# Performance work log

Measured on AMD Instinct MI355X. Metric: run time of the kernel, lower is better.

The kernel has to match this reference:

```python
import jax, jax.numpy as jnp
from jax import lax
import numpy as np

T, N, C, S = 256, 64, 7356, 32
NEG = -1e9  # finite stand-in for -inf (keeps grads clean)


def setup_inputs() -> dict:
    key = jax.random.key(0)
    k1, k2, k3 = jax.random.split(key, 3)
    out = jax.random.normal(k1, (T, N, C), dtype=jnp.float32)
    # PyTorch CTCLoss expects log-probs; the module passes `out` through as-is,
    # so we feed log_softmax'd activations (what the surrounding model produces).
    out = jax.nn.log_softmax(out, axis=-1)
    text = jax.random.randint(k2, (N, S), 1, C)            # labels in [1, C-1], blank=0 excluded
    pre_len = jnp.full((N,), T, dtype=jnp.int64 if jax.config.jax_enable_x64 else jnp.int32)
    lengths = jax.random.randint(k3, (N,), 16, S + 1)       # target lengths in [16, 32]
    return {"out": out, "text": text, "pre_len": pre_len, "lengths": lengths}


def _ctc_loss_mean(logp, targets, input_lengths, target_lengths):
    # logp: [T, N, C] log-probs; targets: [N, S]; lengths: [N]
    Tt, Nn, _ = logp.shape
    Ss = targets.shape[1]
    L = 2 * Ss + 1
    # Extended label sequence: blank, l1, blank, l2, ..., blank
    ext = jnp.zeros((Nn, L), dtype=targets.dtype).at[:, 1::2].set(targets)  # [N, L]
    ext_m2 = jnp.concatenate([jnp.zeros((Nn, 2), dtype=ext.dtype), ext[:, :-2]], axis=1)
    skip = (jnp.arange(L)[None, :] >= 2) & (ext != 0) & (ext != ext_m2)      # [N, L]

    # Gather per-frame log-probs of extended labels: [T, N, L]
    lp_ext = logp[:, jnp.arange(Nn)[:, None], ext]

    alpha0 = jnp.full((Nn, L), NEG, dtype=logp.dtype)
    alpha0 = alpha0.at[:, 0].set(lp_ext[0, :, 0]).at[:, 1].set(lp_ext[0, :, 1])

    negcol1 = jnp.full((Nn, 1), NEG, dtype=logp.dtype)
    negcol2 = jnp.full((Nn, 2), NEG, dtype=logp.dtype)

    def step(alpha, lp_t):
        s1 = jnp.concatenate([negcol1, alpha[:, :-1]], axis=1)
        s2 = jnp.concatenate([negcol2, alpha[:, :-2]], axis=1)
        a = jnp.logaddexp(alpha, s1)
        a = jnp.logaddexp(a, jnp.where(skip, s2, NEG))
        new = a + lp_t
        return new, new

    _, alphas_rest = lax.scan(step, alpha0, lp_ext[1:])
    alphas = jnp.concatenate([alpha0[None], alphas_rest], axis=0)  # [T, N, L]

    n_idx = jnp.arange(Nn)
    a_end = alphas[input_lengths - 1, n_idx]                        # [N, L]
    l_last = 2 * target_lengths                                     # index of final blank
    log_like = jnp.logaddexp(a_end[n_idx, l_last], a_end[n_idx, l_last - 1])
    # reduction='mean': per-sample loss / target_length, then mean over batch
    per = -log_like / target_lengths.astype(logp.dtype)
    return jnp.mean(per)


def reference(out, text, pre_len, lengths):
    loss = _ctc_loss_mean(out, text, pre_len, lengths)
    weight = jnp.square(1.0 - jnp.exp(-loss))
    return weight * loss
```

## Files before the change

### kernel.cpp

```cpp
#include <hip/hip_runtime.h>

#define Tt 256
#define Nn 64
#define Cc 7356
#define Ss 32
#define NEGf (-1.0e9f)
#define LOG2E 1.4426950408889634f
#define LN2   0.6931471805599453f
#define PFD 16
#define HT 128

__device__ __forceinline__ float fexp2(float x) { return __builtin_amdgcn_exp2f(x); }
__device__ __forceinline__ float flog2(float x) { return __builtin_amdgcn_logf(x); }

__device__ __forceinline__ float dpp_shr1(float x, float fallback) {
    int r = __builtin_amdgcn_update_dpp(__float_as_int(fallback), __float_as_int(x),
                                        0x138 , 0xf, 0xf, false);
    return __int_as_float(r);
}
__device__ __forceinline__ float dpp_shl1(float x, float fallback) {
    int r = __builtin_amdgcn_update_dpp(__float_as_int(fallback), __float_as_int(x),
                                        0x130 , 0xf, 0xf, false);
    return __int_as_float(r);
}
__device__ __forceinline__ float bcast(float x, int l) {
    return __int_as_float(__builtin_amdgcn_readlane(__float_as_int(x), l));
}
__device__ __forceinline__ float lse2(float a, float b) {
    float m = fmaxf(a, b);
    return m + flog2(fexp2(a - m) + fexp2(b - m));
}

#define WS_NEED_BYTES (Nn * 132 * 4)

__global__ __launch_bounds__(64) void ctc_fb_kernel(
    const float* __restrict__ logp, const int* __restrict__ text,
    const int* __restrict__ lengths, float* __restrict__ ws)
{
    const int lane = threadIdx.x;
    const int n    = blockIdx.x & (Nn - 1);
    const bool fwd = blockIdx.x < Nn;

    int ch = (lane & 1) ? 0 : text[n * Ss + (lane >> 1)];
    int ch_m2 = __shfl_up(ch, 2, 64);
    int ch_p2 = __shfl_down(ch, 2, 64);
    const bool skipd = (lane >= 2) && !(lane & 1) && (ch != ch_m2);
    const bool skips = !(lane & 1) && (lane <= 61) && (ch != ch_p2);

    const size_t rowbase = (size_t)n * Cc;
    const size_t tstride = (size_t)Nn * Cc;

    float* outv = ws + n * 132 + (fwd ? 0 : 66);

    float stv;
    float st0;

    if (fwd) {
        float lp0 = logp[rowbase + ch] * LOG2E;
        stv = (lane == 0) ? lp0 : NEGf;
        st0 = bcast(lp0, 1);
        float lpb[PFD];
        #pragma unroll
        for (int i = 0; i < PFD; ++i)
            lpb[i] = logp[(size_t)(1 + i) * tstride + rowbase + ch] * LOG2E;
        int t = 1;
        for (int blk = 0; blk < 7; ++blk) {
            #pragma unroll
            for (int j = 0; j < PFD; ++j) {
                float lp = lpb[j];
                int tpf = t + PFD;
                if (tpf <= HT - 1)
                    lpb[j] = logp[(size_t)tpf * tstride + rowbase + ch] * LOG2E;
                float lpblank = bcast(lp, 1);
                float s1 = dpp_shr1(stv, st0);
                float s2 = dpp_shr1(s1, NEGf);
                float s2m = skipd ? s2 : NEGf;
                float m  = fmaxf(fmaxf(stv, s1), s2m);
                float e  = fexp2(stv - m) + fexp2(s1 - m) + fexp2(s2m - m);
                stv = (m + lp) + flog2(e);
                st0 = st0 + lpblank;
                ++t;
            }
        }
        #pragma unroll
        for (int j = 0; j < PFD - 1; ++j) {
            float lp = lpb[j];
            float lpblank = bcast(lp, 1);
            float s1 = dpp_shr1(stv, st0);
            float s2 = dpp_shr1(s1, NEGf);
            float s2m = skipd ? s2 : NEGf;
            float m  = fmaxf(fmaxf(stv, s1), s2m);
            float e  = fexp2(stv - m) + fexp2(s1 - m) + fexp2(s2m - m);
            stv = (m + lp) + flog2(e);
            st0 = st0 + lpblank;
        }
        float s1 = dpp_shr1(stv, st0);
        float s2 = dpp_shr1(s1, NEGf);
        float s2m = skipd ? s2 : NEGf;
        float m  = fmaxf(fmaxf(stv, s1), s2m);
        float e  = fexp2(stv - m) + fexp2(s1 - m) + fexp2(s2m - m);
        outv[1 + lane] = m + flog2(e);
        if (lane == 0) outv[0] = st0;
    } else {
        const int len = lengths[n];
        float lpT = logp[(size_t)(Tt - 1) * tstride + rowbase + ch] * LOG2E;
        int llast = 2 * len;
        stv = (lane == llast - 2 || lane == llast - 1) ? lpT : NEGf;
        st0 = NEGf;
        float lpb[PFD];
        #pragma unroll
        for (int i = 0; i < PFD; ++i)
            lpb[i] = logp[(size_t)(Tt - 2 - i) * tstride + rowbase + ch] * LOG2E;
        int t = Tt - 2;
        for (int blk = 0; blk < 7; ++blk) {
            #pragma unroll
            for (int j = 0; j < PFD; ++j) {
                float lp = lpb[j];
                int tpf = t - PFD;
                if (tpf >= HT)
                    lpb[j] = logp[(size_t)tpf * tstride + rowbase + ch] * LOG2E;
                float lpblank = bcast(lp, 1);
                float b1 = bcast(stv, 0);
                float u1 = dpp_shl1(stv, NEGf);
                float u2 = dpp_shl1(u1, NEGf);
                float u2m = skips ? u2 : NEGf;
                float m  = fmaxf(fmaxf(stv, u1), u2m);
                float e  = fexp2(stv - m) + fexp2(u1 - m) + fexp2(u2m - m);
                float nb = (m + lp) + flog2(e);
                float m2 = fmaxf(st0, b1);
                st0 = (m2 + lpblank) + flog2(fexp2(st0 - m2) + fexp2(b1 - m2));
                stv = nb;
                --t;
            }
        }
        #pragma unroll
        for (int j = 0; j < PFD - 1; ++j) {
            float lp = lpb[j];
            float lpblank = bcast(lp, 1);
            float b1 = bcast(stv, 0);
            float u1 = dpp_shl1(stv, NEGf);
            float u2 = dpp_shl1(u1, NEGf);
            float u2m = skips ? u2 : NEGf;
            float m  = fmaxf(fmaxf(stv, u1), u2m);
            float e  = fexp2(stv - m) + fexp2(u1 - m) + fexp2(u2m - m);
            float nb = (m + lp) + flog2(e);
            float m2 = fmaxf(st0, b1);
            st0 = (m2 + lpblank) + flog2(fexp2(st0 - m2) + fexp2(b1 - m2));
            stv = nb;
        }
        outv[1 + lane] = stv;
        if (lane == 0) outv[0] = st0;
    }
}

__global__ __launch_bounds__(64) void ctc_join_kernel(
    const float* __restrict__ ws, const int* __restrict__ lengths,
    float* __restrict__ out)
{
    const int lane = threadIdx.x;
    const float* va = ws + lane * 132;
    const float* vb = va + 66;
    float acc = NEGf;
    #pragma unroll 5
    for (int s = 0; s <= 64; ++s)
        acc = lse2(acc, va[s] + vb[s]);
    float per = -(acc * LN2) / (float)lengths[lane];
    #pragma unroll
    for (int off = 32; off > 0; off >>= 1)
        per += __shfl_down(per, off, 64);
    if (lane == 0) {
        float loss = per * (1.0f / (float)Nn);
        float w = 1.0f - __expf(-loss);
        out[0] = w * w * loss;
    }
}

__global__ __launch_bounds__(64) void ctc_alpha_kernel(
    const float* __restrict__ logp, const int* __restrict__ text,
    const int* __restrict__ pre_len, const int* __restrict__ lengths,
    float* __restrict__ per_out)
{
    const int n = blockIdx.x; const int lane = threadIdx.x;
    int ch = 0;
    if (lane & 1) ch = text[n * Ss + (lane >> 1)];
    int ch_m2 = __shfl_up(ch, 2, 64);
    bool skip = (lane >= 2) && (ch != 0) && (ch != ch_m2);
    const size_t rowbase = (size_t)n * Cc, tstride = (size_t)Nn * Cc;
    float lp0 = logp[rowbase + ch] * LOG2E;
    float alpha = (lane < 2) ? lp0 : NEGf, alpha64 = NEGf;
    const int stop_t = pre_len[n] - 1;
    float sv = alpha, sv64 = alpha64;
    float lpb[PFD];
    #pragma unroll
    for (int i = 0; i < PFD; ++i)
        lpb[i] = logp[(size_t)(1 + i) * tstride + rowbase + ch] * LOG2E;
#define CTC_STEP(LPREG) { \
        float lp = (LPREG); float lpblank = bcast(lp, 0); float a63 = bcast(alpha, 63); \
        float s1 = dpp_shr1(alpha, NEGf); float s2 = dpp_shr1(s1, NEGf); \
        float s2m = skip ? s2 : NEGf; \
        float m = fmaxf(fmaxf(alpha, s1), s2m); \
        float e = fexp2(alpha - m) + fexp2(s1 - m) + fexp2(s2m - m); \
        float na = (m + lp) + flog2(e); \
        float m2 = fmaxf(alpha64, a63); \
        alpha64 = (m2 + lpblank) + flog2(fexp2(alpha64 - m2) + fexp2(a63 - m2)); \
        alpha = na; if (t == stop_t) { sv = alpha; sv64 = alpha64; } ++t; }
    int t = 1;
    for (int blk = 0; blk < 15; ++blk) {
        #pragma unroll
        for (int j = 0; j < PFD; ++j) {
            float lpj = lpb[j]; int tpf = t + PFD;
            if (tpf < Tt) lpb[j] = logp[(size_t)tpf * tstride + rowbase + ch] * LOG2E;
            CTC_STEP(lpj);
        }
    }
    #pragma unroll
    for (int j = 0; j < PFD - 1; ++j) { CTC_STEP(lpb[j]); }
#undef CTC_STEP
    int len = lengths[n]; int l_last = 2 * len;
    float v1 = __shfl(sv, l_last < 64 ? l_last : 63, 64);
    if (l_last == 64) v1 = sv64;
    float v2 = __shfl(sv, l_last - 1, 64);
    float per = -(lse2(v1, v2) * LN2) / (float)len;
    if (lane == 0) per_out[n] = per;
}

__global__ __launch_bounds__(64) void finalize_kernel(
    const float* __restrict__ per, float* __restrict__ out)
{
    int lane = threadIdx.x;
    float v = per[lane];
    #pragma unroll
    for (int off = 32; off > 0; off >>= 1) v += __shfl_down(v, off, 64);
    if (lane == 0) {
        float loss = v * (1.0f / (float)Nn);
        float w = 1.0f - __expf(-loss);
        out[0] = w * w * loss;
    }
}

extern "C" void kernel_launch(void* const* d_in, const int* in_sizes, int n_in,
                              void* d_out, int out_size, void* d_ws, size_t ws_size,
                              hipStream_t stream) {
    const float* logp    = (const float*)d_in[0];
    const int*   text    = (const int*)d_in[1];
    const int*   pre_len = (const int*)d_in[2];
    const int*   lengths = (const int*)d_in[3];

    if (ws_size >= (size_t)WS_NEED_BYTES) {
        ctc_fb_kernel<<<2 * Nn, 64, 0, stream>>>(logp, text, lengths, (float*)d_ws);
        ctc_join_kernel<<<1, 64, 0, stream>>>((const float*)d_ws, lengths, (float*)d_out);
    } else {
        float* per = (float*)d_ws;
        ctc_alpha_kernel<<<Nn, 64, 0, stream>>>(logp, text, pre_len, lengths, per);
        finalize_kernel<<<1, 64, 0, stream>>>(per, (float*)d_out);
    }
}
```

Measured before the change: 30.71 us.

## Pre-gather extended-label log-probs into compact buffer before forward-backward

Adds a wide parallel gather kernel that reads the per-frame log-probs of each extended label (scaled by log2 e) from the large [T,N,C] tensor into a compact [T,N,64] workspace array. The latency-bound forward/backward recurrence kernels then read coalesced, contiguous rows instead of scattered gathers with long latency. This costs an extra kernel launch and a round trip through a 4 MB workspace, and the recurrence falls back to the old path if the workspace is too small.

```diff
diff --git a/kernel.cpp b/kernel.cpp
--- a/kernel.cpp
+++ b/kernel.cpp
@@ -31,10 +31,24 @@
     return m + flog2(fexp2(a - m) + fexp2(b - m));
 }
 
-#define WS_NEED_BYTES (Nn * 132 * 4)
+#define COMPACT_FLOATS (Tt * Nn * 64)
+#define JV_OFF COMPACT_FLOATS
+#define WS_NEED_BYTES ((COMPACT_FLOATS + Nn * 132) * 4)
+
+__global__ __launch_bounds__(256) void ctc_gather_kernel(
+    const float* __restrict__ logp, const int* __restrict__ text,
+    float* __restrict__ compact)
+{
+    int tid = blockIdx.x * 256 + threadIdx.x;
+    int l = tid & 63;
+    int n = (tid >> 6) & (Nn - 1);
+    int t = tid >> 12;
+    int ch = (l & 1) ? 0 : text[n * Ss + (l >> 1)];
+    compact[tid] = logp[(size_t)t * (Nn * Cc) + (size_t)n * Cc + ch] * LOG2E;
+}
 
 __global__ __launch_bounds__(64) void ctc_fb_kernel(
-    const float* __restrict__ logp, const int* __restrict__ text,
+    const float* __restrict__ compact, const int* __restrict__ text,
     const int* __restrict__ lengths, float* __restrict__ ws)
 {
     const int lane = threadIdx.x;
@@ -47,22 +61,22 @@
     const bool skipd = (lane >= 2) && !(lane & 1) && (ch != ch_m2);
     const bool skips = !(lane & 1) && (lane <= 61) && (ch != ch_p2);
 
-    const size_t rowbase = (size_t)n * Cc;
-    const size_t tstride = (size_t)Nn * Cc;
-
-    float* outv = ws + n * 132 + (fwd ? 0 : 66);
+    const float* base = compact + (size_t)n * 64 + lane;
+    const int rstride = Nn * 64;
+
+    float* outv = ws + JV_OFF + n * 132 + (fwd ? 0 : 66);
 
     float stv;
     float st0;
 
     if (fwd) {
-        float lp0 = logp[rowbase + ch] * LOG2E;
+        float lp0 = base[0];
         stv = (lane == 0) ? lp0 : NEGf;
         st0 = bcast(lp0, 1);
         float lpb[PFD];
         #pragma unroll
         for (int i = 0; i < PFD; ++i)
-            lpb[i] = logp[(size_t)(1 + i) * tstride + rowbase + ch] * LOG2E;
+            lpb[i] = base[(size_t)(1 + i) * rstride];
         int t = 1;
         for (int blk = 0; blk < 7; ++blk) {
             #pragma unroll
@@ -70,7 +84,7 @@
                 float lp = lpb[j];
                 int tpf = t + PFD;
                 if (tpf <= HT - 1)
-                    lpb[j] = logp[(size_t)tpf * tstride + rowbase + ch] * LOG2E;
+                    lpb[j] = base[(size_t)tpf * rstride];
                 float lpblank = bcast(lp, 1);
                 float s1 = dpp_shr1(stv, st0);
                 float s2 = dpp_shr1(s1, NEGf);
@@ -103,14 +117,14 @@
         if (lane == 0) outv[0] = st0;
     } else {
         const int len = lengths[n];
-        float lpT = logp[(size_t)(Tt - 1) * tstride + rowbase + ch] * LOG2E;
+        float lpT = base[(size_t)(Tt - 1) * rstride];
         int llast = 2 * len;
         stv = (lane == llast - 2 || lane == llast - 1) ? lpT : NEGf;
         st0 = NEGf;
         float lpb[PFD];
         #pragma unroll
         for (int i = 0; i < PFD; ++i)
-            lpb[i] = logp[(size_t)(Tt - 2 - i) * tstride + rowbase + ch] * LOG2E;
+            lpb[i] = base[(size_t)(Tt - 2 - i) * rstride];
         int t = Tt - 2;
         for (int blk = 0; blk < 7; ++blk) {
             #pragma unroll
@@ -118,7 +132,7 @@
                 float lp = lpb[j];
                 int tpf = t - PFD;
                 if (tpf >= HT)
-                    lpb[j] = logp[(size_t)tpf * tstride + rowbase + ch] * LOG2E;
+                    lpb[j] = base[(size_t)tpf * rstride];
                 float lpblank = bcast(lp, 1);
                 float b1 = bcast(stv, 0);
                 float u1 = dpp_shl1(stv, NEGf);
@@ -158,7 +172,7 @@
     float* __restrict__ out)
 {
     const int lane = threadIdx.x;
-    const float* va = ws + lane * 132;
+    const float* va = ws + JV_OFF + lane * 132;
     const float* vb = va + 66;
     float acc = NEGf;
     #pragma unroll 5
@@ -247,7 +261,9 @@
     const int*   lengths = (const int*)d_in[3];
 
     if (ws_size >= (size_t)WS_NEED_BYTES) {
-        ctc_fb_kernel<<<2 * Nn, 64, 0, stream>>>(logp, text, lengths, (float*)d_ws);
+        float* compact = (float*)d_ws;
+        ctc_gather_kernel<<<COMPACT_FLOATS / 256, 256, 0, stream>>>(logp, text, compact);
+        ctc_fb_kernel<<<2 * Nn, 64, 0, stream>>>(compact, text, lengths, (float*)d_ws);
         ctc_join_kernel<<<1, 64, 0, stream>>>((const float*)d_ws, lengths, (float*)d_out);
     } else {
         float* per = (float*)d_ws;
```

Result: slower. 33.34 us (+8.6%).
